# Performance work log

Measured on AMD Instinct MI355X. Metric: run time of the kernel, lower is better.

## Reference

```python
import jax, jax.numpy as jnp
import numpy as np
from jax import lax

COND_RATE = 4  # para_cond_downscale_rate
DG = 8        # deformable_groups


def _conv(x, w, b, pad=0, groups=1):
    out = lax.conv_general_dilated(x, w, (1, 1), [(pad, pad), (pad, pad)],
                                   feature_group_count=groups,
                                   dimension_numbers=('NCHW', 'OIHW', 'NCHW'))
    return out + b[None, :, None, None]


def _gn(x, g, b, groups=32, eps=1e-6):
    B, C, H, W = x.shape
    xr = x.reshape(B, groups, C // groups, H * W)
    m = xr.mean(axis=(2, 3), keepdims=True)
    v = ((xr - m) ** 2).mean(axis=(2, 3), keepdims=True)
    xr = (xr - m) * lax.rsqrt(v + eps)
    return xr.reshape(B, C, H, W) * g[None, :, None, None] + b[None, :, None, None]


def _deform_conv2d(x, offset, mask, w, b, dg):
    # x: [B,Cin,H,W], offset: [B,2*dg*9,H,W] (torchvision layout: interleaved y,x per loc),
    # mask: [B,dg*9,H,W], w: [Cout,Cin,3,3]. stride=1, pad=1, dil=1, zero border.
    B, Cin, H, W = x.shape
    K = 9
    Cpg = Cin // dg
    Cout = w.shape[0]
    off = offset.reshape(B, dg, K, 2, H, W)
    ky = (jnp.arange(K) // 3).astype(x.dtype)
    kx = (jnp.arange(K) % 3).astype(x.dtype)
    iy = jnp.arange(H, dtype=x.dtype)
    ix = jnp.arange(W, dtype=x.dtype)
    base_y = iy[None, :, None] - 1.0 + ky[:, None, None]  # [K,H,1]
    base_x = ix[None, None, :] - 1.0 + kx[:, None, None]  # [K,1,W]
    py = off[:, :, :, 0] + base_y[None, None]  # [B,dg,K,H,W]
    px = off[:, :, :, 1] + base_x[None, None]
    y0 = jnp.floor(py)
    x0 = jnp.floor(px)
    ly = py - y0
    lx = px - x0
    xg = x.reshape(B, dg, Cpg, H * W)

    def corner(yc, xc, wt):
        valid = (yc >= 0) & (yc < H) & (xc >= 0) & (xc < W)
        yci = jnp.clip(yc, 0, H - 1).astype(jnp.int32)
        xci = jnp.clip(xc, 0, W - 1).astype(jnp.int32)
        idx = (yci * W + xci).reshape(B, dg, 1, K * H * W)
        v = jnp.take_along_axis(xg, idx, axis=3).reshape(B, dg, Cpg, K, H, W)
        return v * (wt * valid.astype(x.dtype))[:, :, None]

    samp = (corner(y0, x0, (1 - ly) * (1 - lx)) + corner(y0, x0 + 1, (1 - ly) * lx)
            + corner(y0 + 1, x0, ly * (1 - lx)) + corner(y0 + 1, x0 + 1, ly * lx))
    samp = samp * mask.reshape(B, dg, 1, K, H, W)
    wr = w.reshape(Cout, dg, Cpg, K)
    out = jnp.einsum('bgckhw,ogck->bohw', samp, wr)
    return out + b[None, :, None, None]


def setup_inputs() -> dict:
    key = jax.random.key(0)
    ks = jax.random.split(key, 10)
    C = 256
    f32 = jnp.float32
    d = {}
    d['main_feature'] = jax.random.normal(ks[0], (8, C, 64, 64), f32)
    d['condition_feature'] = jax.random.normal(ks[1], (8, C, 16, 16), f32)
    # offset_conv1: 1x1 -> GN -> SiLU -> depthwise 7x7 -> GN -> SiLU -> 1x1
    d['w1'] = jax.random.normal(ks[2], (C, 2 * C, 1, 1), f32) * 0.03
    d['b1'] = jnp.zeros((C,), f32)
    d['g1'] = jnp.ones((C,), f32)
    d['be1'] = jnp.zeros((C,), f32)
    d['w2'] = jax.random.normal(ks[3], (C, 1, 7, 7), f32) * 0.05
    d['b2'] = jnp.zeros((C,), f32)
    d['g2'] = jnp.ones((C,), f32)
    d['be2'] = jnp.zeros((C,), f32)
    d['w3'] = jax.random.normal(ks[4], (C, C, 1, 1), f32) * 0.03
    d['b3'] = jnp.zeros((C,), f32)
    # offset_conv2: 3x3 -> GN -> SiLU
    d['w4'] = jax.random.normal(ks[5], (C, C, 3, 3), f32) * 0.02
    d['b4'] = jnp.zeros((C,), f32)
    d['g3'] = jnp.ones((C,), f32)
    d['be3'] = jnp.zeros((C,), f32)
    # DCNv2Pack conv_offset: 3x3 -> 3*dg*9 = 216 channels (small init -> small offsets)
    d['w_co'] = jax.random.normal(ks[6], (3 * DG * 9, C, 3, 3), f32) * 0.01
    d['b_co'] = jnp.zeros((3 * DG * 9,), f32)
    # DCN main weight
    d['w_dcn'] = jax.random.normal(ks[7], (C, C, 3, 3), f32) * 0.02
    d['b_dcn'] = jnp.zeros((C,), f32)
    return d


def reference(main_feature, condition_feature, w1, b1, g1, be1, w2, b2, g2, be2,
              w3, b3, w4, b4, g3, be3, w_co, b_co, w_dcn, b_dcn):
    B, Cc, h, w_ = condition_feature.shape
    _, Cm, H, W = main_feature.shape
    # note: 2 // cond_downscale_rate == 0 for rate=4, so first resize is identity-sized
    cond = jax.image.resize(condition_feature, (B, Cc, h + 2 // COND_RATE, w_ + 2 // COND_RATE), 'bilinear')
    cond = jax.image.resize(cond, (B, Cc, H, W), 'bilinear')
    f = jnp.concatenate([cond, main_feature], axis=1)
    f = _conv(f, w1, b1)
    f = jax.nn.silu(_gn(f, g1, be1))
    f = _conv(f, w2, b2, pad=3, groups=Cm)  # depthwise 7x7
    f = jax.nn.silu(_gn(f, g2, be2))
    f = _conv(f, w3, b3)
    f = _conv(f, w4, b4, pad=1)
    offset_feat = jax.nn.silu(_gn(f, g3, be3))
    co = _conv(offset_feat, w_co, b_co, pad=1)  # [B, 3*dg*9, H, W]
    o1, o2, m = jnp.split(co, 3, axis=1)
    off = jnp.concatenate([o1, o2], axis=1)     # [B, 2*dg*9, H, W]
    mask = jax.nn.sigmoid(m)
    warp = _deform_conv2d(main_feature, off, mask, w_dcn, b_dcn, DG)
    return (warp, offset_feat)
```

## Files before the change

### kernel.cpp

```cpp
#include <hip/hip_runtime.h>
#include <cstdint>

#define TPB 256

typedef __attribute__((ext_vector_type(8))) short s16x8;
typedef __attribute__((ext_vector_type(4))) short s16x4;
typedef __attribute__((ext_vector_type(4))) float f32x4;

__device__ __forceinline__ float silu_f(float x) { return x / (1.f + __expf(-x)); }

__device__ __forceinline__ short f2bf(float f) {
  union { float f; unsigned u; } v; v.f = f;
  unsigned r = v.u + 0x7fffu + ((v.u >> 16) & 1u);
  return (short)(r >> 16);
}
__device__ __forceinline__ float bf2f(short s) {
  union { unsigned u; float f; } v;
  v.u = ((unsigned)(unsigned short)s) << 16;
  return v.f;
}

__global__ void k_prep_all(const float* __restrict__ w1, const float* __restrict__ w3,
                           const float* __restrict__ w4, const float* __restrict__ wco,
                           const float* __restrict__ wdcn, short* __restrict__ dst) {
  int idx = blockIdx.x * TPB + threadIdx.x;
  if (idx >= 1966080) return;
  const float* w; int Cout, Cin, taps, mode; int local = idx;
  if (idx < 131072)       { w = w1;   Cout = 256; Cin = 512; taps = 1; mode = 0; }
  else if (idx < 196608)  { w = w3;   local -= 131072;  Cout = 256; Cin = 256; taps = 1; mode = 0; }
  else if (idx < 786432)  { w = w4;   local -= 196608;  Cout = 256; Cin = 256; taps = 9; mode = 0; }
  else if (idx < 1376256) { w = wco;  local -= 786432;  Cout = 216; Cin = 256; taps = 9; mode = 0; }
  else                    { w = wdcn; local -= 1376256; Cout = 256; Cin = 256; taps = 9; mode = 1; }
  int j = local & 7;
  int l = (local >> 3) & 63;
  int ot = (local >> 9) & 15;
  int q = local >> 13;
  int tap, cb;
  if (mode == 0) { int ncb = Cin >> 5; tap = q / ncb; cb = q - tap * ncb; }
  else           { tap = q % 9; cb = q / 9; }
  int o = ot * 16 + (l & 15);
  int c = cb * 32 + ((l >> 4) & 3) * 8 + j;
  float v = 0.f;
  if (o < Cout && c < Cin) v = w[((size_t)o * Cin + c) * taps + tap];
  dst[idx] = f2bf(v);
}

__global__ void k_upsample_nhwc(const float* __restrict__ in, short* __restrict__ outA) {
  int idx = blockIdx.x * TPB + threadIdx.x;
  if (idx >= 8 * 4096 * 256) return;
  int c = idx & 255;
  int p = idx >> 8;
  int b = p >> 12;
  int rem = p & 4095;
  int y = rem >> 6, x = rem & 63;
  float sy = (y + 0.5f) * 0.25f - 0.5f;
  float sx = (x + 0.5f) * 0.25f - 0.5f;
  float y0f = floorf(sy), x0f = floorf(sx);
  float ly = sy - y0f, lx = sx - x0f;
  int y0 = (int)y0f, x0 = (int)x0f;
  int y0c = min(15, max(0, y0)), y1c = min(15, max(0, y0 + 1));
  int x0c = min(15, max(0, x0)), x1c = min(15, max(0, x0 + 1));
  const float* src = in + (size_t)(b * 256 + c) * 256;
  float v00 = src[y0c * 16 + x0c], v01 = src[y0c * 16 + x1c];
  float v10 = src[y1c * 16 + x0c], v11 = src[y1c * 16 + x1c];
  float r = (1.f - ly) * ((1.f - lx) * v00 + lx * v01)
          + ly * ((1.f - lx) * v10 + lx * v11);
  outA[(size_t)p * 512 + c] = f2bf(r);
}

__global__ __launch_bounds__(256) void k_main_tr(const float* __restrict__ in,
    short* __restrict__ xbf, short* __restrict__ outA) {
  const int pc = blockIdx.x, ck = blockIdx.y, b = blockIdx.z;
  __shared__ float sl[32][66];
  const int t = threadIdx.x;
  const int pxl = t & 63, cs = t >> 6;
  const float* src = in + (size_t)(b * 256 + ck * 32) * 4096 + pc * 64;
  #pragma unroll
  for (int i = 0; i < 8; ++i) {
    int c = i * 4 + cs;
    sl[c][pxl] = src[(size_t)c * 4096 + pxl];
  }
  __syncthreads();
  const int oct = (t & 3) * 8, px2 = t >> 2;
  s16x8 v;
  #pragma unroll
  for (int j = 0; j < 8; ++j) v[j] = f2bf(sl[oct + j][px2]);
  size_t p = (size_t)b * 4096 + pc * 64 + px2;
  *(s16x8*)(xbf + p * 256 + ck * 32 + oct) = v;
  *(s16x8*)(outA + p * 512 + 256 + ck * 32 + oct) = v;
}

__global__ __launch_bounds__(256) void k_conv2(
    const short* __restrict__ in, int Cin, int Cout, int taps,
    const short* __restrict__ wf, const float* __restrict__ bias,
    short* __restrict__ out, int remap) {
  const int gid = blockIdx.x;
  const int b = gid & 7;
  const int r = gid >> 3;
  const int og = r & 3, yt = r >> 2;
  const int t = threadIdx.x;
  const int wid = t >> 6, l = t & 63;
  const int wo = wid >> 1, wr = wid & 1;
  const int pd = (taps == 9) ? 1 : 0;
  const int rows_in = 2 + 2 * pd;
  const int pxw = 64 + 2 * pd;
  const int ncb = Cin >> 5;
  const int nchunk = Cin >> 6;
  const int ndy = (taps == 9) ? 3 : 1;
  __shared__ __align__(16) short sl[4 * 66 * 68];
  f32x4 acc[2][4];
  #pragma unroll
  for (int i = 0; i < 2; ++i)
    #pragma unroll
    for (int j = 0; j < 4; ++j) acc[i][j] = (f32x4){0.f, 0.f, 0.f, 0.f};
  const int y0g = yt * 2 - pd;
  for (int chunk = 0; chunk < nchunk; ++chunk) {
    __syncthreads();
    {
      const int nun = rows_in * pxw * 8;
      const int c0 = chunk * 64;
      #pragma unroll
      for (int i = 0; i < 9; ++i) {
        int e = t + i * 256;
        if (e < nun) {
          int oct = e & 7;
          int pe = e >> 3;
          int pxs = pe % pxw;
          int row = pe / pxw;
          int yy = y0g + row, xx = pxs - pd;
          s16x8 v = {0, 0, 0, 0, 0, 0, 0, 0};
          if (yy >= 0 && yy < 64 && xx >= 0 && xx < 64)
            v = *(const s16x8*)(in + (size_t)((b * 64 + yy) * 64 + xx) * Cin
                                + c0 + oct * 8);
          *(s16x8*)(sl + (row * 66 + pxs) * 68 + oct * 8) = v;
        }
      }
    }
    __syncthreads();
    #pragma unroll 2
    for (int cb = 0; cb < 2; ++cb) {
      const int qc = chunk * 2 + cb;
      for (int dyi = 0; dyi < ndy; ++dyi) {
        const int lrow = wr + dyi;
        for (int dxi = 0; dxi < ndy; ++dxi) {
          const int tap = (taps == 9) ? dyi * 3 + dxi : 0;
          const int q = tap * ncb + qc;
          s16x8 afr[2];
          #pragma unroll
          for (int i = 0; i < 2; ++i) {
            int ot = og * 4 + wo * 2 + i;
            afr[i] = *(const s16x8*)(wf + (((size_t)q * 16 + ot) * 64 + l) * 8);
          }
          #pragma unroll
          for (int jt = 0; jt < 4; ++jt) {
            int pxi = jt * 16 + (l & 15) + dxi;
            s16x8 bfr = *(const s16x8*)(sl + (lrow * 66 + pxi) * 68
                                        + cb * 32 + (l >> 4) * 8);
            #pragma unroll
            for (int i = 0; i < 2; ++i)
              acc[i][jt] = __builtin_amdgcn_mfma_f32_16x16x32_bf16(
                  afr[i], bfr, acc[i][jt], 0, 0, 0);
          }
        }
      }
    }
  }
  const int y = yt * 2 + wr;
  #pragma unroll
  for (int i = 0; i < 2; ++i) {
    #pragma unroll
    for (int jt = 0; jt < 4; ++jt) {
      int px = jt * 16 + (l & 15);
      int obase = og * 64 + wo * 32 + i * 16 + (l >> 4) * 4;
      size_t pbase = (size_t)((b * 64 + y) * 64 + px) * (remap ? 256 : Cout);
      if (!remap) {
        s16x4 r2;
        #pragma unroll
        for (int rr = 0; rr < 4; ++rr) r2[rr] = f2bf(acc[i][jt][rr] + bias[obase + rr]);
        *(s16x4*)(out + pbase + obase) = r2;
      } else {
        #pragma unroll
        for (int rr = 0; rr < 4; ++rr) {
          int o = obase + rr;
          if (o < Cout) {
            int op;
            if (o < 144) op = (o / 18) * 32 + (o % 18);
            else { int jj = o - 144; op = (jj / 9) * 32 + 18 + (jj % 9); }
            out[pbase + op] = f2bf(acc[i][jt][rr] + bias[o]);
          }
        }
      }
    }
  }
}

__global__ __launch_bounds__(256) void k_gn_stats(const short* __restrict__ io,
    float* __restrict__ parts) {
  const int gid = blockIdx.x;
  const int b = gid & 7;
  const int r = gid >> 3;
  const int ck = r & 7, g = r >> 3;
  const int t = threadIdx.x;
  float s = 0.f, sq = 0.f;
  #pragma unroll
  for (int i = 0; i < 2; ++i) {
    int e = ck * 512 + t + i * 256;
    s16x8 v = *(const s16x8*)(io + (size_t)(b * 4096 + e) * 256 + g * 8);
    #pragma unroll
    for (int j = 0; j < 8; ++j) { float f = bf2f(v[j]); s += f; sq += f * f; }
  }
  #pragma unroll
  for (int off = 32; off > 0; off >>= 1) {
    s += __shfl_down(s, off);
    sq += __shfl_down(sq, off);
  }
  __shared__ float ps[4], pq[4];
  const int wv = t >> 6, lane = t & 63;
  if (lane == 0) { ps[wv] = s; pq[wv] = sq; }
  __syncthreads();
  if (t == 0) {
    parts[gid * 2]     = ps[0] + ps[1] + ps[2] + ps[3];
    parts[gid * 2 + 1] = pq[0] + pq[1] + pq[2] + pq[3];
  }
}

__global__ __launch_bounds__(256) void k_gn_apply(short* __restrict__ io,
    float* __restrict__ f32out, const float* __restrict__ parts,
    const float* __restrict__ gamma, const float* __restrict__ beta) {
  const int gid = blockIdx.x;
  const int b = gid & 7;
  const int r = gid >> 3;
  const int ck = r & 7, g = r >> 3;
  const int t = threadIdx.x;
  float S = 0.f, Q = 0.f;
  #pragma unroll
  for (int i = 0; i < 8; ++i) {
    int gid2 = (((g << 3) | i) << 3) | b;
    S += parts[gid2 * 2];
    Q += parts[gid2 * 2 + 1];
  }
  const float mean = S * (1.f / 32768.f);
  const float var = Q * (1.f / 32768.f) - mean * mean;
  const float rs = rsqrtf(var + 1e-6f);
  float ga[8], bb[8];
  #pragma unroll
  for (int j = 0; j < 8; ++j) {
    ga[j] = gamma[g * 8 + j] * rs;
    bb[j] = beta[g * 8 + j] - mean * ga[j];
  }
  #pragma unroll
  for (int i = 0; i < 2; ++i) {
    int e = ck * 512 + t + i * 256;
    short* ptr = io + (size_t)(b * 4096 + e) * 256 + g * 8;
    s16x8 v = *(const s16x8*)ptr;
    s16x8 r2;
    #pragma unroll
    for (int j = 0; j < 8; ++j) {
      float o = silu_f(bf2f(v[j]) * ga[j] + bb[j]);
      r2[j] = f2bf(o);
      if (f32out) f32out[(size_t)(b * 256 + g * 8 + j) * 4096 + e] = o;
    }
    *(s16x8*)ptr = r2;
  }
}

__global__ __launch_bounds__(256) void k_dw7_nhwc(const short* __restrict__ in,
    const float* __restrict__ w, const float* __restrict__ bias,
    short* __restrict__ out) {
  const int gid = blockIdx.x;
  const int b = gid & 7;
  const int r = gid >> 3;
  const int ck = r & 7, yt = r >> 3;
  const int t = threadIdx.x;
  const int px = t & 63, oc = t >> 6;
  __shared__ __align__(16) short sl[10 * 70 * 40];
  __shared__ float wl[49 * 32];
  for (int e = t; e < 49 * 32; e += TPB) {
    int tap = e >> 5, cc = e & 31;
    wl[tap * 32 + cc] = w[(ck * 32 + cc) * 49 + tap];
  }
  const int y0in = yt * 4 - 3;
  #pragma unroll
  for (int i = 0; i < 11; ++i) {
    int e = t + i * TPB;
    if (e < 2800) {
      int oc2 = e & 3;
      int pe = e >> 2;
      int pxs = pe % 70;
      int row = pe / 70;
      int yy = y0in + row, xx = pxs - 3;
      s16x8 v = {0, 0, 0, 0, 0, 0, 0, 0};
      if (yy >= 0 && yy < 64 && xx >= 0 && xx < 64)
        v = *(const s16x8*)(in + (size_t)((b * 64 + yy) * 64 + xx) * 256
                            + ck * 32 + oc2 * 8);
      *(s16x8*)(sl + (row * 70 + pxs) * 40 + oc2 * 8) = v;
    }
  }
  __syncthreads();
  float acc[4][8];
  {
    float4 b0 = *(const float4*)(bias + ck * 32 + oc * 8);
    float4 b1 = *(const float4*)(bias + ck * 32 + oc * 8 + 4);
    #pragma unroll
    for (int r2 = 0; r2 < 4; ++r2) {
      acc[r2][0] = b0.x; acc[r2][1] = b0.y; acc[r2][2] = b0.z; acc[r2][3] = b0.w;
      acc[r2][4] = b1.x; acc[r2][5] = b1.y; acc[r2][6] = b1.z; acc[r2][7] = b1.w;
    }
  }
  #pragma unroll
  for (int ky = 0; ky < 7; ++ky) {
    #pragma unroll
    for (int kx = 0; kx < 7; ++kx) {
      const float4 w0 = *(const float4*)(wl + (ky * 7 + kx) * 32 + oc * 8);
      const float4 w1 = *(const float4*)(wl + (ky * 7 + kx) * 32 + oc * 8 + 4);
      #pragma unroll
      for (int r2 = 0; r2 < 4; ++r2) {
        s16x8 v = *(const s16x8*)(sl + ((r2 + ky) * 70 + (px + kx)) * 40 + oc * 8);
        acc[r2][0] += bf2f(v[0]) * w0.x; acc[r2][1] += bf2f(v[1]) * w0.y;
        acc[r2][2] += bf2f(v[2]) * w0.z; acc[r2][3] += bf2f(v[3]) * w0.w;
        acc[r2][4] += bf2f(v[4]) * w1.x; acc[r2][5] += bf2f(v[5]) * w1.y;
        acc[r2][6] += bf2f(v[6]) * w1.z; acc[r2][7] += bf2f(v[7]) * w1.w;
      }
    }
  }
  #pragma unroll
  for (int r2 = 0; r2 < 4; ++r2) {
    int y = yt * 4 + r2;
    s16x8 o;
    #pragma unroll
    for (int j = 0; j < 8; ++j) o[j] = f2bf(acc[r2][j]);
    *(s16x8*)(out + (size_t)((b * 64 + y) * 64 + px) * 256 + ck * 32 + oc * 8) = o;
  }
}

__global__ __launch_bounds__(256) void k_dcn_nhwc(const short* __restrict__ x,
    const short* __restrict__ co, const short* __restrict__ wf,
    const float* __restrict__ bias, float* __restrict__ out) {
  const int gid = blockIdx.x;
  const int b = gid & 7;
  const int r = gid >> 3;
  const int ph = r & 1, y = r >> 1;
  const int t = threadIdx.x;
  const int wid = t >> 6, l = t & 63;
  const int px0 = ph * 32;
  __shared__ __align__(16) short s2[9 * 32 * 40];
  __shared__ unsigned swt[288 * 9];
  f32x4 acc[4][2];
  #pragma unroll
  for (int i = 0; i < 4; ++i)
    #pragma unroll
    for (int j = 0; j < 2; ++j) acc[i][j] = (f32x4){0.f, 0.f, 0.f, 0.f};
  const short* xb = x + (size_t)b * 4096 * 256;
  for (int g = 0; g < 8; ++g) {
    __syncthreads();
    #pragma unroll
    for (int i = 0; i < 2; ++i) {
      int e2 = t + i * 256;
      if (e2 < 288) {
        int pxl = e2 & 31, k = e2 >> 5;
        int px = px0 + pxl;
        const short* cp = co + (size_t)(b * 4096 + y * 64 + px) * 256 + g * 32;
        float offy = bf2f(cp[2 * k]);
        float offx = bf2f(cp[2 * k + 1]);
        float mlog = bf2f(cp[18 + k]);
        float mv = 1.f / (1.f + __expf(-mlog));
        float py = offy + (float)(y - 1 + k / 3);
        float pxf = offx + (float)(px - 1 + k % 3);
        float y0f = floorf(py), x0f = floorf(pxf);
        float ly = py - y0f, lx = pxf - x0f;
        int y0 = (int)y0f, x0 = (int)x0f;
        int y1 = y0 + 1, x1 = x0 + 1;
        float fy0 = (y0 >= 0 && y0 < 64) ? 1.f : 0.f;
        float fy1 = (y1 >= 0 && y1 < 64) ? 1.f : 0.f;
        float fx0 = (x0 >= 0 && x0 < 64) ? 1.f : 0.f;
        float fx1 = (x1 >= 0 && x1 < 64) ? 1.f : 0.f;
        float w00 = (1.f - ly) * (1.f - lx) * fy0 * fx0 * mv;
        float w01 = (1.f - ly) * lx * fy0 * fx1 * mv;
        float w10 = ly * (1.f - lx) * fy1 * fx0 * mv;
        float w11 = ly * lx * fy1 * fx1 * mv;
        int y0c = min(63, max(0, y0)), y1c = min(63, max(0, y1));
        int x0c = min(63, max(0, x0)), x1c = min(63, max(0, x1));
        unsigned* wp = swt + e2 * 9;
        wp[0] = __float_as_uint(w00);
        wp[1] = __float_as_uint(w01);
        wp[2] = __float_as_uint(w10);
        wp[3] = __float_as_uint(w11);
        wp[4] = (unsigned)((y0c * 64 + x0c) * 256);
        wp[5] = (unsigned)((y0c * 64 + x1c) * 256);
        wp[6] = (unsigned)((y1c * 64 + x0c) * 256);
        wp[7] = (unsigned)((y1c * 64 + x1c) * 256);
      }
    }
    __syncthreads();
    #pragma unroll
    for (int i = 0; i < 5; ++i) {
      int e = t + i * 256;
      if (e < 1152) {
        int oct = e & 3, pxl = (e >> 2) & 31, k = e >> 7;
        const unsigned* wp = swt + (k * 32 + pxl) * 9;
        float w00 = __uint_as_float(wp[0]);
        float w01 = __uint_as_float(wp[1]);
        float w10 = __uint_as_float(wp[2]);
        float w11 = __uint_as_float(wp[3]);
        const short* xc = xb + g * 32 + oct * 8;
        s16x8 c00 = *(const s16x8*)(xc + wp[4]);
        s16x8 c01 = *(const s16x8*)(xc + wp[5]);
        s16x8 c10 = *(const s16x8*)(xc + wp[6]);
        s16x8 c11 = *(const s16x8*)(xc + wp[7]);
        s16x8 pk;
        #pragma unroll
        for (int cc = 0; cc < 8; ++cc) {
          float v = w00 * bf2f(c00[cc]) + w01 * bf2f(c01[cc])
                  + w10 * bf2f(c10[cc]) + w11 * bf2f(c11[cc]);
          pk[cc] = f2bf(v);
        }
        *(s16x8*)(s2 + (k * 32 + pxl) * 40 + oct * 8) = pk;
      }
    }
    __syncthreads();
    #pragma unroll
    for (int k = 0; k < 9; ++k) {
      const int q = g * 9 + k;
      s16x8 afr[4], bfr[2];
      #pragma unroll
      for (int i = 0; i < 4; ++i)
        afr[i] = *(const s16x8*)(wf + (((size_t)q * 16 + wid * 4 + i) * 64 + l) * 8);
      #pragma unroll
      for (int jt = 0; jt < 2; ++jt)
        bfr[jt] = *(const s16x8*)(s2 + (k * 32 + jt * 16 + (l & 15)) * 40 + (l >> 4) * 8);
      #pragma unroll
      for (int i = 0; i < 4; ++i)
        #pragma unroll
        for (int jt = 0; jt < 2; ++jt)
          acc[i][jt] = __builtin_amdgcn_mfma_f32_16x16x32_bf16(
              afr[i], bfr[jt], acc[i][jt], 0, 0, 0);
    }
  }
  #pragma unroll
  for (int i = 0; i < 4; ++i) {
    int obase = wid * 64 + i * 16 + (l >> 4) * 4;
    #pragma unroll
    for (int jt = 0; jt < 2; ++jt) {
      int pxo = px0 + jt * 16 + (l & 15);
      #pragma unroll
      for (int rr = 0; rr < 4; ++rr) {
        int o = obase + rr;
        out[(((size_t)b * 256 + o) * 64 + y) * 64 + pxo] = acc[i][jt][rr] + bias[o];
      }
    }
  }
}

extern "C" void kernel_launch(void* const* d_in, const int* in_sizes, int n_in,
                              void* d_out, int out_size, void* d_ws, size_t ws_size,
                              hipStream_t stream) {
  const float* main_f = (const float*)d_in[0];
  const float* cond   = (const float*)d_in[1];
  const float* w1  = (const float*)d_in[2];
  const float* b1  = (const float*)d_in[3];
  const float* g1  = (const float*)d_in[4];
  const float* be1 = (const float*)d_in[5];
  const float* w2  = (const float*)d_in[6];
  const float* b2  = (const float*)d_in[7];
  const float* g2  = (const float*)d_in[8];
  const float* be2 = (const float*)d_in[9];
  const float* w3  = (const float*)d_in[10];
  const float* b3  = (const float*)d_in[11];
  const float* w4  = (const float*)d_in[12];
  const float* b4  = (const float*)d_in[13];
  const float* g3  = (const float*)d_in[14];
  const float* be3 = (const float*)d_in[15];
  const float* w_co  = (const float*)d_in[16];
  const float* b_co  = (const float*)d_in[17];
  const float* w_dcn = (const float*)d_in[18];
  const float* b_dcn = (const float*)d_in[19];

  float* out = (float*)d_out;
  float* warp_out = out;
  float* offset_feat = out + 8388608;

  short* ws = (short*)d_ws;
  short* bufA  = ws;
  short* Bb    = bufA + 16777216;
  short* xbf   = Bb + 8388608;
  short* wfall = xbf + 8388608;
  short* wf1   = wfall;
  short* wf3   = wf1 + 131072;
  short* wf4   = wf3 + 65536;
  short* wfco  = wf4 + 589824;
  short* wfdcn = wfco + 589824;
  float* gparts = (float*)(wfdcn + 589824);

  auto cdiv = [](int a, int b) { return (a + b - 1) / b; };

  k_prep_all<<<cdiv(1966080, TPB), TPB, 0, stream>>>(w1, w3, w4, w_co, w_dcn, wfall);

  k_upsample_nhwc<<<cdiv(8 * 4096 * 256, TPB), TPB, 0, stream>>>(cond, bufA);
  dim3 gtr(64, 8, 8);
  k_main_tr<<<gtr, TPB, 0, stream>>>(main_f, xbf, bufA);

  k_conv2<<<1024, TPB, 0, stream>>>(bufA, 512, 256, 1, wf1, b1, Bb, 0);
  k_gn_stats<<<2048, TPB, 0, stream>>>(Bb, gparts);
  k_gn_apply<<<2048, TPB, 0, stream>>>(Bb, nullptr, gparts, g1, be1);
  k_dw7_nhwc<<<1024, TPB, 0, stream>>>(Bb, w2, b2, bufA);
  k_gn_stats<<<2048, TPB, 0, stream>>>(bufA, gparts);
  k_gn_apply<<<2048, TPB, 0, stream>>>(bufA, nullptr, gparts, g2, be2);
  k_conv2<<<1024, TPB, 0, stream>>>(bufA, 256, 256, 1, wf3, b3, Bb, 0);
  k_conv2<<<1024, TPB, 0, stream>>>(Bb, 256, 256, 9, wf4, b4, bufA, 0);
  k_gn_stats<<<2048, TPB, 0, stream>>>(bufA, gparts);
  k_gn_apply<<<2048, TPB, 0, stream>>>(bufA, offset_feat, gparts, g3, be3);
  k_conv2<<<1024, TPB, 0, stream>>>(bufA, 256, 216, 9, wfco, b_co, Bb, 1);
  k_dcn_nhwc<<<1024, TPB, 0, stream>>>(xbf, Bb, wfdcn, b_dcn, warp_out);
}
```

Measured before the change: 446.3 us.

## Fold GroupNorm+SiLU apply into consumer conv input loads

```diff
diff --git a/kernel.cpp b/kernel.cpp
--- a/kernel.cpp
+++ b/kernel.cpp
@@ -93,7 +93,7 @@
 __global__ __launch_bounds__(256) void k_conv2(
     const short* __restrict__ in, int Cin, int Cout, int taps,
     const short* __restrict__ wf, const float* __restrict__ bias,
-    short* __restrict__ out, int remap) {
+    short* __restrict__ out, int remap, const float2* __restrict__ gab) {
   const int gid = blockIdx.x;
   const int b = gid & 7;
   const int r = gid >> 3;
@@ -129,9 +129,18 @@
           int row = pe / pxw;
           int yy = y0g + row, xx = pxs - pd;
           s16x8 v = {0, 0, 0, 0, 0, 0, 0, 0};
-          if (yy >= 0 && yy < 64 && xx >= 0 && xx < 64)
+          if (yy >= 0 && yy < 64 && xx >= 0 && xx < 64) {
             v = *(const s16x8*)(in + (size_t)((b * 64 + yy) * 64 + xx) * Cin
                                 + c0 + oct * 8);
+            if (gab) {
+              const float2* gp = gab + b * 256 + c0 + oct * 8;
+              #pragma unroll
+              for (int j = 0; j < 8; ++j) {
+                float2 ab = gp[j];
+                v[j] = f2bf(silu_f(bf2f(v[j]) * ab.x + ab.y));
+              }
+            }
+          }
           *(s16x8*)(sl + (row * 66 + pxs) * 68 + oct * 8) = v;
         }
       }
@@ -224,6 +233,27 @@
   }
 }
 
+__global__ __launch_bounds__(256) void k_gn_fin(const float* __restrict__ parts,
+    const float* __restrict__ gamma, const float* __restrict__ beta,
+    float2* __restrict__ gab) {
+  int idx = blockIdx.x * TPB + threadIdx.x;
+  if (idx >= 2048) return;
+  const int b = idx >> 8, c = idx & 255, g = c >> 3;
+  float S = 0.f, Q = 0.f;
+  #pragma unroll
+  for (int i = 0; i < 8; ++i) {
+    int gid2 = (((g << 3) | i) << 3) | b;
+    S += parts[gid2 * 2];
+    Q += parts[gid2 * 2 + 1];
+  }
+  const float mean = S * (1.f / 32768.f);
+  const float var = Q * (1.f / 32768.f) - mean * mean;
+  const float rs = rsqrtf(var + 1e-6f);
+  float ga = gamma[c] * rs;
+  float bb = beta[c] - mean * ga;
+  gab[idx] = make_float2(ga, bb);
+}
+
 __global__ __launch_bounds__(256) void k_gn_apply(short* __restrict__ io,
     float* __restrict__ f32out, const float* __restrict__ parts,
     const float* __restrict__ gamma, const float* __restrict__ beta) {
@@ -266,7 +296,7 @@
 
 __global__ __launch_bounds__(256) void k_dw7_nhwc(const short* __restrict__ in,
     const float* __restrict__ w, const float* __restrict__ bias,
-    short* __restrict__ out) {
+    short* __restrict__ out, const float2* __restrict__ gab) {
   const int gid = blockIdx.x;
   const int b = gid & 7;
   const int r = gid >> 3;
@@ -290,9 +320,16 @@
       int row = pe / 70;
       int yy = y0in + row, xx = pxs - 3;
       s16x8 v = {0, 0, 0, 0, 0, 0, 0, 0};
-      if (yy >= 0 && yy < 64 && xx >= 0 && xx < 64)
+      if (yy >= 0 && yy < 64 && xx >= 0 && xx < 64) {
         v = *(const s16x8*)(in + (size_t)((b * 64 + yy) * 64 + xx) * 256
                             + ck * 32 + oc2 * 8);
+        const float2* gp = gab + b * 256 + ck * 32 + oc2 * 8;
+        #pragma unroll
+        for (int j = 0; j < 8; ++j) {
+          float2 ab = gp[j];
+          v[j] = f2bf(silu_f(bf2f(v[j]) * ab.x + ab.y));
+        }
+      }
       *(s16x8*)(sl + (row * 70 + pxs) * 40 + oc2 * 8) = v;
     }
   }
@@ -490,6 +527,7 @@
   short* wfco  = wf4 + 589824;
   short* wfdcn = wfco + 589824;
   float* gparts = (float*)(wfdcn + 589824);
+  float2* gab   = (float2*)(gparts + 4096);
 
   auto cdiv = [](int a, int b) { return (a + b - 1) / b; };
 
@@ -499,16 +537,16 @@
   dim3 gtr(64, 8, 8);
   k_main_tr<<<gtr, TPB, 0, stream>>>(main_f, xbf, bufA);
 
-  k_conv2<<<1024, TPB, 0, stream>>>(bufA, 512, 256, 1, wf1, b1, Bb, 0);
+  k_conv2<<<1024, TPB, 0, stream>>>(bufA, 512, 256, 1, wf1, b1, Bb, 0, nullptr);
   k_gn_stats<<<2048, TPB, 0, stream>>>(Bb, gparts);
-  k_gn_apply<<<2048, TPB, 0, stream>>>(Bb, nullptr, gparts, g1, be1);
-  k_dw7_nhwc<<<1024, TPB, 0, stream>>>(Bb, w2, b2, bufA);
+  k_gn_fin<<<8, TPB, 0, stream>>>(gparts, g1, be1, gab);
+  k_dw7_nhwc<<<1024, TPB, 0, stream>>>(Bb, w2, b2, bufA, gab);
   k_gn_stats<<<2048, TPB, 0, stream>>>(bufA, gparts);
-  k_gn_apply<<<2048, TPB, 0, stream>>>(bufA, nullptr, gparts, g2, be2);
-  k_conv2<<<1024, TPB, 0, stream>>>(bufA, 256, 256, 1, wf3, b3, Bb, 0);
-  k_conv2<<<1024, TPB, 0, stream>>>(Bb, 256, 256, 9, wf4, b4, bufA, 0);
+  k_gn_fin<<<8, TPB, 0, stream>>>(gparts, g2, be2, gab);
+  k_conv2<<<1024, TPB, 0, stream>>>(bufA, 256, 256, 1, wf3, b3, Bb, 0, gab);
+  k_conv2<<<1024, TPB, 0, stream>>>(Bb, 256, 256, 9, wf4, b4, bufA, 0, nullptr);
   k_gn_stats<<<2048, TPB, 0, stream>>>(bufA, gparts);
   k_gn_apply<<<2048, TPB, 0, stream>>>(bufA, offset_feat, gparts, g3, be3);
-  k_conv2<<<1024, TPB, 0, stream>>>(bufA, 256, 216, 9, wfco, b_co, Bb, 1);
+  k_conv2<<<1024, TPB, 0, stream>>>(bufA, 256, 216, 9, wfco, b_co, Bb, 1, nullptr);
   k_dcn_nhwc<<<1024, TPB, 0, stream>>>(xbf, Bb, wfdcn, b_dcn, warp_out);
 }
```

Result: slower. 460.2 us (+3.1%).
